# Performance work log

Measured on AMD Instinct MI355X. Metric: run time of the kernel, lower is better.

## Reference

```python
import jax, jax.numpy as jnp
import numpy as np

B, H, W, C = 4, 64, 64, 256
CQK = C // 8  # squeeze_times = 8


def setup_inputs() -> dict:
    key = jax.random.key(0)
    ks = jax.random.split(key, 7)
    s = 0.02
    return {
        "x": jax.random.normal(ks[0], (B, H, W, C), dtype=jnp.float32),
        "Wq": jax.random.normal(ks[1], (C, CQK), dtype=jnp.float32) * s,
        "bq": jnp.zeros((CQK,), dtype=jnp.float32),
        "Wk": jax.random.normal(ks[2], (C, CQK), dtype=jnp.float32) * s,
        "bk": jnp.zeros((CQK,), dtype=jnp.float32),
        "Wv": jax.random.normal(ks[3], (C, C), dtype=jnp.float32) * s,
        "bv": jnp.zeros((C,), dtype=jnp.float32),
        "gamma": jnp.zeros((), dtype=jnp.float32) + 0.5,  # nonzero so residual path is exercised
    }


def reference(x, Wq, bq, Wk, bk, Wv, bv, gamma):
    b, h, w, c = x.shape
    n = h * w
    # 1x1 convs == per-pixel dense layers
    q = x @ Wq + bq                       # (B,H,W,CQK)
    k = x @ Wk + bk                       # (B,H,W,CQK)
    v = x @ Wv + bv                       # (B,H,W,C)
    pq = q.reshape(b, n, -1)              # (B,N,CQK)
    pk = k.reshape(b, n, -1)              # (B,N,CQK)
    pv = v.reshape(b, n, -1)              # (B,N,C)
    # energy[b,i,j] = <q_i, k_j>, unscaled (as in original)
    energy = jnp.einsum('bid,bjd->bij', pq, pk)   # (B,N,N)
    attention = jax.nn.softmax(energy, axis=-1)   # softmax over last axis
    # out = proj_value (B,C,N) @ attention^T -> out[b,c,i] = sum_j v[b,j,c]*att[b,i,j]
    out = jnp.einsum('bjc,bij->bic', pv, attention)  # (B,N,C)
    out = out.reshape(b, h, w, c)
    return out * gamma + x, attention
```

## Files before the change

kernel.cpp:

```cpp
#include <hip/hip_runtime.h>

typedef __bf16 bf16_t;
typedef bf16_t bf16x8 __attribute__((ext_vector_type(8)));
typedef float f32x4 __attribute__((ext_vector_type(4)));

#define MFMA16(a, b, c) __builtin_amdgcn_mfma_f32_16x16x32_bf16(a, b, c, 0, 0, 0)

static __device__ __forceinline__ unsigned short f2bf(float f) {
  unsigned int u = __builtin_bit_cast(unsigned int, f);
  unsigned int r = (u + 0x7fffu + ((u >> 16) & 1u)) >> 16;
  return (unsigned short)r;
}

__global__ void prep_kernel(const float* __restrict__ x, const float* __restrict__ Wq,
                            const float* __restrict__ Wk, const float* __restrict__ Wv,
                            unsigned short* __restrict__ xb, unsigned short* __restrict__ Wt) {
  int tid = blockIdx.x * 256 + threadIdx.x;
  int stride = gridDim.x * 256;
  const float4* x4 = (const float4*)x;
  ushort4* xb4 = (ushort4*)xb;
  for (int i = tid; i < (4 * 4096 * 256) / 4; i += stride) {
    float4 v = x4[i];
    ushort4 o;
    o.x = f2bf(v.x); o.y = f2bf(v.y); o.z = f2bf(v.z); o.w = f2bf(v.w);
    xb4[i] = o;
  }
  for (int i = tid; i < 320 * 256; i += stride) {
    int n = i >> 8, k = i & 255;
    float v = (n < 32) ? Wq[k * 32 + n] : (n < 64) ? Wk[k * 32 + (n - 32)] : Wv[k * 256 + (n - 64)];
    Wt[i] = f2bf(v);
  }
}

__global__ __launch_bounds__(256) void qkv_kernel(
    const unsigned short* __restrict__ xb, const unsigned short* __restrict__ Wt,
    const float* __restrict__ bq, const float* __restrict__ bk, const float* __restrict__ bv,
    unsigned short* __restrict__ Qb, unsigned short* __restrict__ Kb,
    unsigned short* __restrict__ Vt) {
  __shared__ unsigned short wbuf[320 * 40];
  const int t = threadIdx.x;
  const int w = t >> 6, l = t & 63;
  const int lc = l & 15, lg = l >> 4;
  const int arow = blockIdx.x * 64 + w * 16 + lc;

  f32x4 acc[20];
#pragma unroll
  for (int i = 0; i < 20; i++) acc[i] = (f32x4){0.f, 0.f, 0.f, 0.f};

  for (int kk = 0; kk < 256; kk += 32) {
    __syncthreads();
#pragma unroll
    for (int i = 0; i < 5; i++) {
      int u = t + i * 256;
      int n = u >> 2, q = u & 3;
      *reinterpret_cast<bf16x8*>(&wbuf[n * 40 + q * 8]) =
          *reinterpret_cast<const bf16x8*>(&Wt[n * 256 + kk + q * 8]);
    }
    __syncthreads();
    bf16x8 af = *reinterpret_cast<const bf16x8*>(&xb[arow * 256 + kk + lg * 8]);
#pragma unroll
    for (int nt = 0; nt < 20; nt++) {
      bf16x8 bf = *reinterpret_cast<const bf16x8*>(&wbuf[(nt * 16 + lc) * 40 + lg * 8]);
      acc[nt] = MFMA16(af, bf, acc[nt]);
    }
  }
  const int orow = blockIdx.x * 64 + w * 16 + lg * 4;
#pragma unroll
  for (int nt = 0; nt < 20; nt++) {
    int co = nt * 16 + lc;
    if (co < 64) {
#pragma unroll
      for (int r = 0; r < 4; r++) {
        int R = orow + r;
        float v = acc[nt][r];
        if (co < 32) Qb[R * 32 + co] = f2bf(v + bq[co]);
        else Kb[R * 32 + (co - 32)] = f2bf(v + bk[co - 32]);
      }
    } else {
      int c = co - 64;
      int bb = orow >> 12, j = orow & 4095;
      ushort4 o;
      o.x = f2bf(acc[nt][0] + bv[c]);
      o.y = f2bf(acc[nt][1] + bv[c]);
      o.z = f2bf(acc[nt][2] + bv[c]);
      o.w = f2bf(acc[nt][3] + bv[c]);
      *reinterpret_cast<ushort4*>(
          &Vt[(((size_t)(bb * 128 + (j >> 5))) * 256 + c) * 32 + (j & 31)]) = o;
    }
  }
}

__global__ __launch_bounds__(256) void attn_kernel(
    const unsigned short* __restrict__ Qb, const unsigned short* __restrict__ Kb,
    const unsigned short* __restrict__ Vt, float* __restrict__ pout,
    float* __restrict__ att) {
  __shared__ unsigned short vbuf[2][256 * 40];
  __shared__ unsigned short pbuf[2][64 * 40];

  const int t = threadIdx.x;
  const int w = t >> 6, l = t & 63;
  const int lc = l & 15, lg = l >> 4;
  const int b = blockIdx.x >> 7;
  const int rb = (blockIdx.x >> 1) & 63;
  const int half = blockIdx.x & 1;
  const int r0 = rb * 64;

  const unsigned short* Kbase = Kb + (size_t)b * 4096 * 32;
  const unsigned short* Vbase = Vt + (size_t)b * 128 * 8192;
  float* attb = att + (size_t)b * 4096 * 4096;

  auto loadK = [&](int ct) {
    return *reinterpret_cast<const bf16x8*>(&Kbase[(ct * 16 + lc) * 32 + lg * 8]);
  };

  bf16x8 aq = *reinterpret_cast<const bf16x8*>(&Qb[((size_t)b * 4096 + r0 + w * 16 + lc) * 32 + lg * 8]);
  const f32x4 zero = {0.f, 0.f, 0.f, 0.f};

  float s[4] = {0.f, 0.f, 0.f, 0.f};
  bf16x8 k0 = loadK(0), k1 = loadK(1), k2 = loadK(2), k3 = loadK(3);
  for (int ct = 0; ct < 256; ct += 4) {
    f32x4 d0 = MFMA16(aq, k0, zero); k0 = loadK(ct + 4);
    f32x4 d1 = MFMA16(aq, k1, zero); k1 = loadK(ct + 5);
    f32x4 d2 = MFMA16(aq, k2, zero); k2 = loadK(ct + 6);
    f32x4 d3 = MFMA16(aq, k3, zero); k3 = loadK(ct + 7);
#pragma unroll
    for (int r = 0; r < 4; r++)
      s[r] += __expf(d0[r] - 8.f) + __expf(d1[r] - 8.f) + __expf(d2[r] - 8.f) +
              __expf(d3[r] - 8.f);
  }
#pragma unroll
  for (int off = 1; off < 16; off <<= 1) {
#pragma unroll
    for (int r = 0; r < 4; r++) s[r] += __shfl_xor(s[r], off, 16);
  }
  float rinv[4];
#pragma unroll
  for (int r = 0; r < 4; r++) rinv[r] = 1.f / s[r];

  f32x4 acc[4][4];
#pragma unroll
  for (int i = 0; i < 4; i++)
#pragma unroll
    for (int j = 0; j < 4; j++) acc[i][j] = zero;

  auto stageLoad = [&](int jc, bf16x8* r) {
#pragma unroll
    for (int i = 0; i < 4; i++)
      r[i] = *reinterpret_cast<const bf16x8*>(&Vbase[(size_t)jc * 8192 + (t + i * 256) * 8]);
  };
  auto stageWrite = [&](unsigned short* buf, const bf16x8* r) {
#pragma unroll
    for (int i = 0; i < 4; i++) {
      int u = t + i * 256, c = u >> 2, q = u & 3;
      *reinterpret_cast<bf16x8*>(&buf[c * 40 + q * 8]) = r[i];
    }
  };

  const int jc0 = half * 64;
  bf16x8 vn[4];
  stageLoad(jc0, vn);
  bf16x8 kn0 = loadK(jc0 * 2), kn1 = loadK(jc0 * 2 + 1);

  int cur = 0;
  for (int i = 0; i < 64; i++) {
    const int jc = jc0 + i;
    f32x4 d0 = MFMA16(aq, kn0, zero);
    f32x4 d1 = MFMA16(aq, kn1, zero);
    stageWrite(vbuf[cur], vn);
    if (i < 63) {
      stageLoad(jc + 1, vn);
      kn0 = loadK((jc + 1) * 2);
      kn1 = loadK((jc + 1) * 2 + 1);
    }
    unsigned short* pb = pbuf[cur];
#pragma unroll
    for (int r = 0; r < 4; r++) {
      float p0 = __expf(d0[r] - 8.f) * rinv[r];
      float p1 = __expf(d1[r] - 8.f) * rinv[r];
      int grow = r0 + w * 16 + lg * 4 + r;
      size_t ai = (size_t)grow * 4096 + jc * 32;
      __builtin_nontemporal_store(p0, &attb[ai + lc]);
      __builtin_nontemporal_store(p1, &attb[ai + 16 + lc]);
      pb[(w * 16 + lg * 4 + r) * 40 + lc] = f2bf(p0);
      pb[(w * 16 + lg * 4 + r) * 40 + 16 + lc] = f2bf(p1);
    }
    __syncthreads();
    const unsigned short* vb = vbuf[cur];
    const unsigned short* pbc = pbuf[cur];
    bf16x8 pa[4];
#pragma unroll
    for (int rg = 0; rg < 4; rg++)
      pa[rg] = *reinterpret_cast<const bf16x8*>(&pbc[(rg * 16 + lc) * 40 + lg * 8]);
#pragma unroll
    for (int ct = 0; ct < 4; ct++) {
      bf16x8 bvv = *reinterpret_cast<const bf16x8*>(&vb[(w * 64 + ct * 16 + lc) * 40 + lg * 8]);
#pragma unroll
      for (int rg = 0; rg < 4; rg++) acc[rg][ct] = MFMA16(pa[rg], bvv, acc[rg][ct]);
    }
    cur ^= 1;
  }

  float* po = pout + (size_t)half * 4 * 4096 * 256;
#pragma unroll
  for (int rg = 0; rg < 4; rg++) {
#pragma unroll
    for (int ct = 0; ct < 4; ct++) {
#pragma unroll
      for (int r = 0; r < 4; r++) {
        size_t oi = ((size_t)b * 4096 + r0 + rg * 16 + lg * 4 + r) * 256 + w * 64 + ct * 16 + lc;
        po[oi] = acc[rg][ct][r];
      }
    }
  }
}

__global__ void reduce_kernel(const float* __restrict__ p0, const float* __restrict__ p1,
                              const float* __restrict__ x, const float* __restrict__ gptr,
                              float* __restrict__ out) {
  const float gamma = *gptr;
  int tid = blockIdx.x * 256 + threadIdx.x;
  int stride = gridDim.x * 256;
  const float4* a = (const float4*)p0;
  const float4* c = (const float4*)p1;
  const float4* xv = (const float4*)x;
  float4* o = (float4*)out;
  for (int i = tid; i < (4 * 4096 * 256) / 4; i += stride) {
    float4 va = a[i], vc = c[i], vx = xv[i];
    float4 r;
    r.x = (va.x + vc.x) * gamma + vx.x;
    r.y = (va.y + vc.y) * gamma + vx.y;
    r.z = (va.z + vc.z) * gamma + vx.z;
    r.w = (va.w + vc.w) * gamma + vx.w;
    o[i] = r;
  }
}

extern "C" void kernel_launch(void* const* d_in, const int* in_sizes, int n_in, void* d_out,
                              int out_size, void* d_ws, size_t ws_size, hipStream_t stream) {
  const float* x = (const float*)d_in[0];
  const float* Wq = (const float*)d_in[1];
  const float* bq = (const float*)d_in[2];
  const float* Wk = (const float*)d_in[3];
  const float* bk = (const float*)d_in[4];
  const float* Wv = (const float*)d_in[5];
  const float* bv = (const float*)d_in[6];
  const float* gm = (const float*)d_in[7];
  float* out = (float*)d_out;
  float* att = out + (size_t)4 * 4096 * 256;

  char* ws = (char*)d_ws;
  unsigned short* xb = (unsigned short*)(ws);
  unsigned short* Wt = (unsigned short*)(ws + 8388608);
  unsigned short* Qb = (unsigned short*)(ws + 8552448);
  unsigned short* Kb = (unsigned short*)(ws + 9601024);
  unsigned short* Vt = (unsigned short*)(ws + 10649600);
  float* pout = (float*)(ws + 19038208);

  prep_kernel<<<2048, 256, 0, stream>>>(x, Wq, Wk, Wv, xb, Wt);
  qkv_kernel<<<256, 256, 0, stream>>>(xb, Wt, bq, bk, bv, Qb, Kb, Vt);
  attn_kernel<<<512, 256, 0, stream>>>(Qb, Kb, Vt, pout, att);
  reduce_kernel<<<2048, 256, 0, stream>>>(pout, pout + (size_t)4 * 4096 * 256, x, gm, out);
}
```

Measured before the change: 387.4 us.

## Split softmax denominator into separate kernel and stage attention stores through LDS

The per-row softmax denominator, previously recomputed redundantly by both half-blocks of attn_kernel, moves into a new denom_kernel that writes reciprocal sums to workspace. attn_kernel loads them instead. attn_kernel also stages fp32 probabilities in shared memory so each thread writes 16-byte vectorized nontemporal stores of contiguous row segments, replacing scattered 4-byte stores. This adds a kernel launch and more LDS usage, which may lower occupancy.

```diff
diff --git a/kernel.cpp b/kernel.cpp
--- a/kernel.cpp
+++ b/kernel.cpp
@@ -90,12 +90,53 @@
   }
 }
 
+__global__ __launch_bounds__(256) void denom_kernel(const unsigned short* __restrict__ Qb,
+                                                    const unsigned short* __restrict__ Kb,
+                                                    float* __restrict__ rinvg) {
+  const int t = threadIdx.x;
+  const int w = t >> 6, l = t & 63;
+  const int lc = l & 15, lg = l >> 4;
+  const int b = blockIdx.x >> 6;
+  const int r0 = (blockIdx.x & 63) * 64;
+
+  const unsigned short* Kbase = Kb + (size_t)b * 4096 * 32;
+  auto loadK = [&](int ct) {
+    return *reinterpret_cast<const bf16x8*>(&Kbase[(ct * 16 + lc) * 32 + lg * 8]);
+  };
+  bf16x8 aq =
+      *reinterpret_cast<const bf16x8*>(&Qb[((size_t)b * 4096 + r0 + w * 16 + lc) * 32 + lg * 8]);
+  const f32x4 zero = {0.f, 0.f, 0.f, 0.f};
+
+  float s[4] = {0.f, 0.f, 0.f, 0.f};
+  bf16x8 k0 = loadK(0), k1 = loadK(1), k2 = loadK(2), k3 = loadK(3);
+  for (int ct = 0; ct < 256; ct += 4) {
+    f32x4 d0 = MFMA16(aq, k0, zero); k0 = loadK(ct + 4);
+    f32x4 d1 = MFMA16(aq, k1, zero); k1 = loadK(ct + 5);
+    f32x4 d2 = MFMA16(aq, k2, zero); k2 = loadK(ct + 6);
+    f32x4 d3 = MFMA16(aq, k3, zero); k3 = loadK(ct + 7);
+#pragma unroll
+    for (int r = 0; r < 4; r++)
+      s[r] += __expf(d0[r] - 8.f) + __expf(d1[r] - 8.f) + __expf(d2[r] - 8.f) +
+              __expf(d3[r] - 8.f);
+  }
+#pragma unroll
+  for (int off = 1; off < 16; off <<= 1) {
+#pragma unroll
+    for (int r = 0; r < 4; r++) s[r] += __shfl_xor(s[r], off, 16);
+  }
+  if (lc == 0) {
+#pragma unroll
+    for (int r = 0; r < 4; r++) rinvg[(size_t)b * 4096 + r0 + w * 16 + lg * 4 + r] = 1.f / s[r];
+  }
+}
+
 __global__ __launch_bounds__(256) void attn_kernel(
     const unsigned short* __restrict__ Qb, const unsigned short* __restrict__ Kb,
-    const unsigned short* __restrict__ Vt, float* __restrict__ pout,
-    float* __restrict__ att) {
+    const unsigned short* __restrict__ Vt, const float* __restrict__ rinvg,
+    float* __restrict__ pout, float* __restrict__ att) {
   __shared__ unsigned short vbuf[2][256 * 40];
   __shared__ unsigned short pbuf[2][64 * 40];
+  __shared__ float pfb[2][64 * 36];
 
   const int t = threadIdx.x;
   const int w = t >> 6, l = t & 63;
@@ -113,29 +154,12 @@
     return *reinterpret_cast<const bf16x8*>(&Kbase[(ct * 16 + lc) * 32 + lg * 8]);
   };
 
-  bf16x8 aq = *reinterpret_cast<const bf16x8*>(&Qb[((size_t)b * 4096 + r0 + w * 16 + lc) * 32 + lg * 8]);
+  bf16x8 aq =
+      *reinterpret_cast<const bf16x8*>(&Qb[((size_t)b * 4096 + r0 + w * 16 + lc) * 32 + lg * 8]);
   const f32x4 zero = {0.f, 0.f, 0.f, 0.f};
 
-  float s[4] = {0.f, 0.f, 0.f, 0.f};
-  bf16x8 k0 = loadK(0), k1 = loadK(1), k2 = loadK(2), k3 = loadK(3);
-  for (int ct = 0; ct < 256; ct += 4) {
-    f32x4 d0 = MFMA16(aq, k0, zero); k0 = loadK(ct + 4);
-    f32x4 d1 = MFMA16(aq, k1, zero); k1 = loadK(ct + 5);
-    f32x4 d2 = MFMA16(aq, k2, zero); k2 = loadK(ct + 6);
-    f32x4 d3 = MFMA16(aq, k3, zero); k3 = loadK(ct + 7);
-#pragma unroll
-    for (int r = 0; r < 4; r++)
-      s[r] += __expf(d0[r] - 8.f) + __expf(d1[r] - 8.f) + __expf(d2[r] - 8.f) +
-              __expf(d3[r] - 8.f);
-  }
-#pragma unroll
-  for (int off = 1; off < 16; off <<= 1) {
-#pragma unroll
-    for (int r = 0; r < 4; r++) s[r] += __shfl_xor(s[r], off, 16);
-  }
-  float rinv[4];
-#pragma unroll
-  for (int r = 0; r < 4; r++) rinv[r] = 1.f / s[r];
+  float4 rv = *reinterpret_cast<const float4*>(&rinvg[(size_t)b * 4096 + r0 + w * 16 + lg * 4]);
+  float rinv[4] = {rv.x, rv.y, rv.z, rv.w};
 
   f32x4 acc[4][4];
 #pragma unroll
@@ -160,6 +184,8 @@
   bf16x8 vn[4];
   stageLoad(jc0, vn);
   bf16x8 kn0 = loadK(jc0 * 2), kn1 = loadK(jc0 * 2 + 1);
+
+  const int srow = t >> 3, sc0 = (t & 7) * 4;
 
   int cur = 0;
   for (int i = 0; i < 64; i++) {
@@ -173,18 +199,27 @@
       kn1 = loadK((jc + 1) * 2 + 1);
     }
     unsigned short* pb = pbuf[cur];
+    float* pf = pfb[cur];
 #pragma unroll
     for (int r = 0; r < 4; r++) {
       float p0 = __expf(d0[r] - 8.f) * rinv[r];
       float p1 = __expf(d1[r] - 8.f) * rinv[r];
-      int grow = r0 + w * 16 + lg * 4 + r;
-      size_t ai = (size_t)grow * 4096 + jc * 32;
-      __builtin_nontemporal_store(p0, &attb[ai + lc]);
-      __builtin_nontemporal_store(p1, &attb[ai + 16 + lc]);
-      pb[(w * 16 + lg * 4 + r) * 40 + lc] = f2bf(p0);
-      pb[(w * 16 + lg * 4 + r) * 40 + 16 + lc] = f2bf(p1);
+      int lr = w * 16 + lg * 4 + r;
+      pf[lr * 36 + lc] = p0;
+      pf[lr * 36 + 16 + lc] = p1;
+      pb[lr * 40 + lc] = f2bf(p0);
+      pb[lr * 40 + 16 + lc] = f2bf(p1);
     }
     __syncthreads();
+    {
+      const float* pfc = pfb[cur];
+      f32x4 v0 = *reinterpret_cast<const f32x4*>(&pfc[srow * 36 + sc0]);
+      f32x4 v1 = *reinterpret_cast<const f32x4*>(&pfc[(srow + 32) * 36 + sc0]);
+      size_t a0 = (size_t)(r0 + srow) * 4096 + jc * 32 + sc0;
+      size_t a1 = (size_t)(r0 + srow + 32) * 4096 + jc * 32 + sc0;
+      __builtin_nontemporal_store(v0, reinterpret_cast<f32x4*>(&attb[a0]));
+      __builtin_nontemporal_store(v1, reinterpret_cast<f32x4*>(&attb[a1]));
+    }
     const unsigned short* vb = vbuf[cur];
     const unsigned short* pbc = pbuf[cur];
     bf16x8 pa[4];
@@ -254,10 +289,12 @@
   unsigned short* Qb = (unsigned short*)(ws + 8552448);
   unsigned short* Kb = (unsigned short*)(ws + 9601024);
   unsigned short* Vt = (unsigned short*)(ws + 10649600);
-  float* pout = (float*)(ws + 19038208);
+  float* rinvg = (float*)(ws + 19038208);
+  float* pout = (float*)(ws + 19103744);
 
   prep_kernel<<<2048, 256, 0, stream>>>(x, Wq, Wk, Wv, xb, Wt);
   qkv_kernel<<<256, 256, 0, stream>>>(xb, Wt, bq, bk, bv, Qb, Kb, Vt);
-  attn_kernel<<<512, 256, 0, stream>>>(Qb, Kb, Vt, pout, att);
+  denom_kernel<<<256, 256, 0, stream>>>(Qb, Kb, rinvg);
+  attn_kernel<<<512, 256, 0, stream>>>(Qb, Kb, Vt, rinvg, pout, att);
   reduce_kernel<<<2048, 256, 0, stream>>>(pout, pout + (size_t)4 * 4096 * 256, x, gm, out);
 }
```

After: 395.9 us. 1.02x slower.
